# Kernel optimization log

Measured on AMD Instinct MI355X. Metric: run time of the kernel, lower is better.

Reference implementation:

```python
import jax, jax.numpy as jnp
import numpy as np


def _cdist_p2(x, y):
    # x: [B, N, D], y: [B, M, D] -> [B, N, M] euclidean distances
    x2 = jnp.sum(x * x, axis=-1, keepdims=True)          # [B, N, 1]
    y2 = jnp.sum(y * y, axis=-1, keepdims=True)          # [B, M, 1]
    xy = jnp.einsum('bnd,bmd->bnm', x, y)                # [B, N, M]
    d2 = x2 + jnp.swapaxes(y2, -1, -2) - 2.0 * xy
    return jnp.sqrt(jnp.maximum(d2, 0.0))


def setup_inputs() -> dict:
    key = jax.random.key(0)
    kx, ky = jax.random.split(key)
    B, N, M, D = 8, 8192, 8192, 64
    x = jax.random.normal(kx, (B, N, D), dtype=jnp.float32)
    y = jax.random.normal(ky, (B, M, D), dtype=jnp.float32)
    return {"x": x, "y": y}


def reference(x, y):
    # relative_distances: [B, N, M]
    rd = _cdist_p2(x, y)
    M = rd.shape[-1]
    a = jnp.min(rd, axis=-1)            # [B, N] nearest y for each x
    b = jnp.min(rd, axis=-2)            # [B, M] nearest x for each y
    loss_per_batch = jnp.sum(a, axis=-1) + jnp.sum(b, axis=-1)  # [B]
    return jnp.mean(loss_per_batch) / M
```

## Files before the change

kernel.cpp:

```cpp
#include <hip/hip_runtime.h>
#include <cstdint>
#include <cstddef>

typedef unsigned short u16;
typedef __attribute__((ext_vector_type(8))) short short8;
typedef __attribute__((ext_vector_type(8))) u16 ushort8;
typedef __attribute__((ext_vector_type(4))) float float4_t;

#define BB 8
#define NN 8192
#define DD 64
#define NTILES 64
#define TILE_SHORTS 8192

__device__ inline u16 f32_to_bf16(float f) {
  unsigned u = __float_as_uint(f);
  u += 0x7FFFu + ((u >> 16) & 1u);
  return (u16)(u >> 16);
}

__device__ inline unsigned enc_ord(float f) {
  unsigned u = __float_as_uint(f);
  return (u & 0x80000000u) ? ~u : (u | 0x80000000u);
}
__device__ inline float dec_ord(unsigned u) {
  return __uint_as_float((u & 0x80000000u) ? (u & 0x7fffffffu) : ~u);
}

__global__ __launch_bounds__(256) void pre_kernel(
    const float* __restrict__ x, const float* __restrict__ y,
    u16* __restrict__ xs, u16* __restrict__ ys,
    float* __restrict__ x2h, float* __restrict__ y2h,
    unsigned* __restrict__ colmax_u, const int use_part)
{
  const int bid = blockIdx.x;
  const int tid = threadIdx.x;

  if (!use_part && bid < 256) colmax_u[(bid << 8) | tid] = 0u;

  const bool isY = bid >= 1024;
  const float* src = isY ? y : x;
  u16* dst = isY ? ys : xs;
  float* s2 = isY ? y2h : x2h;

  const int row = ((bid & 1023) << 6) | (tid >> 2);
  const int kq  = tid & 3;

  const float4* rp = (const float4*)(src + (size_t)row * DD + kq * 16);
  float buf[16];
  float ss = 0.f;
#pragma unroll
  for (int k = 0; k < 4; ++k) {
    float4 f = rp[k];
    buf[4*k+0] = f.x; buf[4*k+1] = f.y; buf[4*k+2] = f.z; buf[4*k+3] = f.w;
    ss += f.x*f.x + f.y*f.y + f.z*f.z + f.w*f.w;
  }
  ss += __shfl_xor(ss, 1);
  ss += __shfl_xor(ss, 2);
  if (kq == 0) s2[row] = 0.5f * ss;

  const int b  = row >> 13;
  const int n  = row & (NN - 1);
  const int nt = n >> 7;
  const int I  = (n >> 4) & 7;
  const int rl = n & 15;
  const int s  = kq >> 1;
  const int qq0 = (kq & 1) * 2;
  u16* tb = dst + (size_t)((b << 6) | nt) * TILE_SHORTS;
#pragma unroll
  for (int t = 0; t < 2; ++t) {
    ushort8 o;
#pragma unroll
    for (int j = 0; j < 8; ++j) o[j] = f32_to_bf16(buf[t*8 + j]);
    *(ushort8*)(tb + (I*2 + s)*512 + ((qq0 + t)*16 + rl)*8) = o;
  }
}

__global__ __launch_bounds__(256, 2) void main_kernel(
    const u16* __restrict__ xs, const u16* __restrict__ ys,
    const float* __restrict__ x2h, const float* __restrict__ y2h,
    float* __restrict__ a_min, float* __restrict__ colpart,
    unsigned* __restrict__ colmax_u, const int use_part)
{
  __shared__ float rowbuf[4][128];

  const int bid = blockIdx.x;
  const int b   = bid & 7;
  const int nt  = bid >> 3;
  const int tid = threadIdx.x;
  const int w = tid >> 6, lane = tid & 63;
  const int l15 = lane & 15, q = lane >> 4;
  const int n0 = nt << 7;

  const u16* xs_tile = xs + (size_t)((b << 6) | nt) * TILE_SHORTS;
  short8 afr[8][2];
#pragma unroll
  for (int i = 0; i < 8; ++i)
#pragma unroll
    for (int s = 0; s < 2; ++s)
      afr[i][s] = *(const short8*)(xs_tile + (i*2 + s)*512 + lane*8);

  float4_t negx2[8];
  const float* x2b = x2h + b*NN + n0;
#pragma unroll
  for (int i = 0; i < 8; ++i) {
    float4_t v = *(const float4_t*)(x2b + i*16 + q*4);
    negx2[i] = {-v[0], -v[1], -v[2], -v[3]};
  }

  float rowmax[8][4];
#pragma unroll
  for (int i = 0; i < 8; ++i)
#pragma unroll
    for (int r = 0; r < 4; ++r) rowmax[i][r] = -3.0e38f;

  const float* y2b = y2h + b*NN;
  const u16* ys_b  = ys + (size_t)(b << 6) * TILE_SHORTS;
  float* colp      = colpart + (size_t)((b << 6) | nt) * NN;
  unsigned* colu   = colmax_u + b*NN;

  short8 bcur[2][2];
  float y2cur[2];
#pragma unroll
  for (int j = 0; j < 2; ++j) {
#pragma unroll
    for (int s = 0; s < 2; ++s)
      bcur[j][s] = *(const short8*)(ys_b + ((2*w + j)*2 + s)*512 + lane*8);
    y2cur[j] = y2b[w*32 + j*16 + l15];
  }

  for (int mt = 0; mt < NTILES; ++mt) {
    const int mtn = (mt + 1 < NTILES) ? (mt + 1) : 0;
    short8 bnext[2][2];
    float y2next[2];
    const u16* g = ys_b + (size_t)mtn * TILE_SHORTS;
#pragma unroll
    for (int j = 0; j < 2; ++j) {
#pragma unroll
      for (int s = 0; s < 2; ++s)
        bnext[j][s] = *(const short8*)(g + ((2*w + j)*2 + s)*512 + lane*8);
      y2next[j] = y2b[mtn*128 + w*32 + j*16 + l15];
    }

    float cmax[2];
#pragma unroll
    for (int j = 0; j < 2; ++j) {
      float4_t acc[8];
#pragma unroll
      for (int i = 0; i < 8; ++i)
        acc[i] = __builtin_amdgcn_mfma_f32_16x16x32_bf16(afr[i][0], bcur[j][0], negx2[i], 0, 0, 0);
#pragma unroll
      for (int i = 0; i < 8; ++i)
        acc[i] = __builtin_amdgcn_mfma_f32_16x16x32_bf16(afr[i][1], bcur[j][1], acc[i], 0, 0, 0);

      float m01 = fmaxf(fmaxf(acc[0][0], acc[0][1]), fmaxf(acc[0][2], acc[0][3]));
#pragma unroll
      for (int i = 1; i < 8; ++i) {
        float mi = fmaxf(fmaxf(acc[i][0], acc[i][1]), fmaxf(acc[i][2], acc[i][3]));
        m01 = fmaxf(m01, mi);
      }
      cmax[j] = m01;

      const float y2j = y2cur[j];
#pragma unroll
      for (int i = 0; i < 8; ++i)
#pragma unroll
        for (int r = 0; r < 4; ++r)
          rowmax[i][r] = fmaxf(rowmax[i][r], acc[i][r] - y2j);
    }

#pragma unroll
    for (int j = 0; j < 2; ++j) {
      cmax[j] = fmaxf(cmax[j], __shfl_xor(cmax[j], 16));
      cmax[j] = fmaxf(cmax[j], __shfl_xor(cmax[j], 32));
    }
    float cv = (q & 1) ? cmax[1] : cmax[0];
    const int m = (mt << 7) + w*32 + q*16 + l15;
    if (q < 2) {
      if (use_part) colp[m] = cv;
      else          atomicMax(&colu[m], enc_ord(cv));
    }

#pragma unroll
    for (int j = 0; j < 2; ++j) {
#pragma unroll
      for (int s = 0; s < 2; ++s) bcur[j][s] = bnext[j][s];
      y2cur[j] = y2next[j];
    }
  }

#pragma unroll
  for (int i = 0; i < 8; ++i)
#pragma unroll
    for (int r = 0; r < 4; ++r) {
      float v = rowmax[i][r];
      v = fmaxf(v, __shfl_xor(v, 1));
      v = fmaxf(v, __shfl_xor(v, 2));
      v = fmaxf(v, __shfl_xor(v, 4));
      v = fmaxf(v, __shfl_xor(v, 8));
      rowmax[i][r] = v;
    }
  if (l15 == 0) {
#pragma unroll
    for (int i = 0; i < 8; ++i)
#pragma unroll
      for (int r = 0; r < 4; ++r)
        rowbuf[w][i*16 + q*4 + r] = rowmax[i][r];
  }
  __syncthreads();
  if (tid < 128) {
    float v = fmaxf(fmaxf(rowbuf[0][tid], rowbuf[1][tid]),
                    fmaxf(rowbuf[2][tid], rowbuf[3][tid]));
    a_min[b*NN + n0 + tid] = sqrtf(fmaxf(-2.f * v, 0.f));
  }
}

__global__ __launch_bounds__(256) void reduce_kernel(
    const float* __restrict__ colpart, const unsigned* __restrict__ colmax_u,
    const float* __restrict__ y2h, const float* __restrict__ a_min,
    float* __restrict__ partials, const int use_part)
{
  const int bid = blockIdx.x;
  const int tid = threadIdx.x;
  const int g = bid*256 + tid;
  const int b = g >> 13, m = g & (NN - 1);

  float vc;
  if (use_part) {
    vc = -3.0e38f;
#pragma unroll 8
    for (int nt = 0; nt < 64; ++nt)
      vc = fmaxf(vc, colpart[(size_t)((b << 6) | nt) * NN + m]);
  } else {
    vc = dec_ord(colmax_u[g]);
  }
  float s = sqrtf(fmaxf(2.f*(y2h[g] - vc), 0.f))
          + a_min[g];

#pragma unroll
  for (int d = 1; d < 64; d <<= 1) s += __shfl_xor(s, d);
  __shared__ float wsum[4];
  if ((tid & 63) == 0) wsum[tid >> 6] = s;
  __syncthreads();
  if (tid == 0) partials[bid] = wsum[0] + wsum[1] + wsum[2] + wsum[3];
}

__global__ void final_kernel(const float* __restrict__ partials, float* __restrict__ out) {
  const int tid = threadIdx.x;
  float s = partials[tid];
#pragma unroll
  for (int d = 1; d < 64; d <<= 1) s += __shfl_xor(s, d);
  __shared__ float wsum[4];
  if ((tid & 63) == 0) wsum[tid >> 6] = s;
  __syncthreads();
  if (tid == 0) out[0] = (wsum[0] + wsum[1] + wsum[2] + wsum[3]) * (1.0f / 65536.0f);
}

extern "C" void kernel_launch(void* const* d_in, const int* in_sizes, int n_in,
                              void* d_out, int out_size, void* d_ws, size_t ws_size,
                              hipStream_t stream) {
  const float* x = (const float*)d_in[0];
  const float* y = (const float*)d_in[1];
  float* out = (float*)d_out;

  char* p = (char*)d_ws;
  u16* xs = (u16*)p;            p += (size_t)512 * 16384;
  u16* ys = (u16*)p;            p += (size_t)512 * 16384;
  float* x2h = (float*)p;       p += (size_t)65536 * 4;
  float* y2h = (float*)p;       p += (size_t)65536 * 4;
  float* a_min = (float*)p;     p += (size_t)65536 * 4;
  float* partials = (float*)p;  p += 4096;
  char* tail = p;
  float* colpart = (float*)tail;
  unsigned* colmax_u = (unsigned*)tail;
  const size_t need_part = (size_t)(tail - (char*)d_ws) + (size_t)512 * 8192 * 4;
  const int use_part = (ws_size >= need_part) ? 1 : 0;

  pre_kernel<<<dim3(2048), dim3(256), 0, stream>>>(x, y, xs, ys, x2h, y2h,
                                                   colmax_u, use_part);
  main_kernel<<<dim3(512), dim3(256), 0, stream>>>(xs, ys, x2h, y2h, a_min,
                                                   colpart, colmax_u, use_part);
  reduce_kernel<<<dim3(256), dim3(256), 0, stream>>>(colpart, colmax_u, y2h,
                                                     a_min, partials, use_part);
  final_kernel<<<dim3(1), dim3(256), 0, stream>>>(partials, out);
}
```

Baseline: 168.8 us.

## Stage pre-kernel tiles through LDS and fold final reduction into atomics

The pre-kernel now loads a whole 128-row tile with coalesced float4 reads into padded LDS, then computes the half squared norms and writes the bf16 fragment layout as contiguous 16-byte stores per lane. This replaces the scattered stores of the old per-row mapping and uses half as many blocks. The separate final reduction kernel is removed: each reduce block atomically adds its scaled partial sum into the output, which the pre-kernel zeroes. This saves one launch but makes the float summation order nondeterministic.

```diff
diff --git a/kernel.cpp b/kernel.cpp
--- a/kernel.cpp
+++ b/kernel.cpp
@@ -12,6 +12,7 @@
 #define DD 64
 #define NTILES 64
 #define TILE_SHORTS 8192
+#define LDS_STRIDE 68
 
 __device__ inline u16 f32_to_bf16(float f) {
   unsigned u = __float_as_uint(f);
@@ -31,48 +32,58 @@
     const float* __restrict__ x, const float* __restrict__ y,
     u16* __restrict__ xs, u16* __restrict__ ys,
     float* __restrict__ x2h, float* __restrict__ y2h,
-    unsigned* __restrict__ colmax_u, const int use_part)
+    unsigned* __restrict__ colmax_u, float* __restrict__ out,
+    const int use_part)
 {
+  __shared__ float stage[128 * LDS_STRIDE];
+
   const int bid = blockIdx.x;
   const int tid = threadIdx.x;
 
   if (!use_part && bid < 256) colmax_u[(bid << 8) | tid] = 0u;
-
-  const bool isY = bid >= 1024;
-  const float* src = isY ? y : x;
-  u16* dst = isY ? ys : xs;
-  float* s2 = isY ? y2h : x2h;
-
-  const int row = ((bid & 1023) << 6) | (tid >> 2);
-  const int kq  = tid & 3;
-
-  const float4* rp = (const float4*)(src + (size_t)row * DD + kq * 16);
-  float buf[16];
-  float ss = 0.f;
-#pragma unroll
-  for (int k = 0; k < 4; ++k) {
-    float4 f = rp[k];
-    buf[4*k+0] = f.x; buf[4*k+1] = f.y; buf[4*k+2] = f.z; buf[4*k+3] = f.w;
-    ss += f.x*f.x + f.y*f.y + f.z*f.z + f.w*f.w;
-  }
-  ss += __shfl_xor(ss, 1);
-  ss += __shfl_xor(ss, 2);
-  if (kq == 0) s2[row] = 0.5f * ss;
-
-  const int b  = row >> 13;
-  const int n  = row & (NN - 1);
-  const int nt = n >> 7;
-  const int I  = (n >> 4) & 7;
-  const int rl = n & 15;
-  const int s  = kq >> 1;
-  const int qq0 = (kq & 1) * 2;
-  u16* tb = dst + (size_t)((b << 6) | nt) * TILE_SHORTS;
-#pragma unroll
-  for (int t = 0; t < 2; ++t) {
-    ushort8 o;
-#pragma unroll
-    for (int j = 0; j < 8; ++j) o[j] = f32_to_bf16(buf[t*8 + j]);
-    *(ushort8*)(tb + (I*2 + s)*512 + ((qq0 + t)*16 + rl)*8) = o;
+  if (bid == 0 && tid == 0) out[0] = 0.f;
+
+  const bool isY = bid >= 512;
+  const int t = bid & 511;
+  const float* src = (isY ? y : x) + (size_t)t * (128 * DD);
+  u16* dst = (isY ? ys : xs) + (size_t)t * TILE_SHORTS;
+  float* s2 = (isY ? y2h : x2h) + t * 128;
+
+#pragma unroll
+  for (int c = 0; c < 8; ++c) {
+    const int idx = c * 256 + tid;
+    float4 f = ((const float4*)src)[idx];
+    const int r = idx >> 4, kc = idx & 15;
+    *(float4*)&stage[r * LDS_STRIDE + kc * 4] = f;
+  }
+  __syncthreads();
+
+  {
+    const int r = tid >> 1, half = tid & 1;
+    const float* rp = &stage[r * LDS_STRIDE + half * 32];
+    float ss = 0.f;
+#pragma unroll
+    for (int k = 0; k < 8; ++k) {
+      float4 f = *(const float4*)&rp[k * 4];
+      ss += f.x*f.x + f.y*f.y + f.z*f.z + f.w*f.w;
+    }
+    ss += __shfl_xor(ss, 1);
+    if (half == 0) s2[r] = 0.5f * ss;
+  }
+
+  {
+    const int w = tid >> 6, lane = tid & 63;
+    const int qq = lane >> 4, rl = lane & 15;
+#pragma unroll
+    for (int u = 0; u < 4; ++u) {
+      const int chunk = w * 4 + u;
+      const int I = chunk >> 1, s = chunk & 1;
+      const float* rp = &stage[(I*16 + rl) * LDS_STRIDE + s*32 + qq*8];
+      ushort8 o;
+#pragma unroll
+      for (int j = 0; j < 8; ++j) o[j] = f32_to_bf16(rp[j]);
+      *(ushort8*)(dst + chunk*512 + lane*8) = o;
+    }
   }
 }
 
@@ -218,7 +229,7 @@
 __global__ __launch_bounds__(256) void reduce_kernel(
     const float* __restrict__ colpart, const unsigned* __restrict__ colmax_u,
     const float* __restrict__ y2h, const float* __restrict__ a_min,
-    float* __restrict__ partials, const int use_part)
+    float* __restrict__ out, const int use_part)
 {
   const int bid = blockIdx.x;
   const int tid = threadIdx.x;
@@ -242,18 +253,8 @@
   __shared__ float wsum[4];
   if ((tid & 63) == 0) wsum[tid >> 6] = s;
   __syncthreads();
-  if (tid == 0) partials[bid] = wsum[0] + wsum[1] + wsum[2] + wsum[3];
-}
-
-__global__ void final_kernel(const float* __restrict__ partials, float* __restrict__ out) {
-  const int tid = threadIdx.x;
-  float s = partials[tid];
-#pragma unroll
-  for (int d = 1; d < 64; d <<= 1) s += __shfl_xor(s, d);
-  __shared__ float wsum[4];
-  if ((tid & 63) == 0) wsum[tid >> 6] = s;
-  __syncthreads();
-  if (tid == 0) out[0] = (wsum[0] + wsum[1] + wsum[2] + wsum[3]) * (1.0f / 65536.0f);
+  if (tid == 0)
+    atomicAdd(out, (wsum[0] + wsum[1] + wsum[2] + wsum[3]) * (1.0f / 65536.0f));
 }
 
 extern "C" void kernel_launch(void* const* d_in, const int* in_sizes, int n_in,
@@ -269,18 +270,16 @@
   float* x2h = (float*)p;       p += (size_t)65536 * 4;
   float* y2h = (float*)p;       p += (size_t)65536 * 4;
   float* a_min = (float*)p;     p += (size_t)65536 * 4;
-  float* partials = (float*)p;  p += 4096;
   char* tail = p;
   float* colpart = (float*)tail;
   unsigned* colmax_u = (unsigned*)tail;
   const size_t need_part = (size_t)(tail - (char*)d_ws) + (size_t)512 * 8192 * 4;
   const int use_part = (ws_size >= need_part) ? 1 : 0;
 
-  pre_kernel<<<dim3(2048), dim3(256), 0, stream>>>(x, y, xs, ys, x2h, y2h,
-                                                   colmax_u, use_part);
+  pre_kernel<<<dim3(1024), dim3(256), 0, stream>>>(x, y, xs, ys, x2h, y2h,
+                                                   colmax_u, out, use_part);
   main_kernel<<<dim3(512), dim3(256), 0, stream>>>(xs, ys, x2h, y2h, a_min,
                                                    colpart, colmax_u, use_part);
   reduce_kernel<<<dim3(256), dim3(256), 0, stream>>>(colpart, colmax_u, y2h,
-                                                     a_min, partials, use_part);
-  final_kernel<<<dim3(1), dim3(256), 0, stream>>>(partials, out);
-}
+                                                     a_min, out, use_part);
+}
```

After: 167.0 us. No clear change (-1.1%).
